# Kernel tuning notes

Measured on AMD Instinct MI355X. Metric: run time of the kernel, lower is better.

The kernel has to match this reference:

```python
import jax, jax.numpy as jnp
import numpy as np

B, N, D = 1, 2048, 2048
H, DH, DR, MP = 16, 128, 64, 4
LOCAL = H * DH // MP  # per-shard qkv width
ATTN_MASK_VALUE = -1e10
LN_EPS = 1e-5


def setup_inputs() -> dict:
    key = jax.random.key(0)
    ks = jax.random.split(key, 5)
    s = 0.02
    return {
        "x": jax.random.normal(ks[0], (B, N, D), jnp.float32),
        "ln_scale": jnp.ones((D,), jnp.float32),
        "ln_offset": jnp.zeros((D,), jnp.float32),
        "w_qkv": jax.random.normal(ks[1], (D, 3 * H * DH), jnp.float32) * s,
        "w_attn_out": jax.random.normal(ks[2], (H * DH, D), jnp.float32) * s,
        "w_ff_in": jax.random.normal(ks[3], (D, 4 * D), jnp.float32) * s,
        "b_ff_in": jnp.zeros((4 * D,), jnp.float32),
        "w_ff_out": jax.random.normal(ks[4], (4 * D, D), jnp.float32) * s,
        "b_ff_out": jnp.zeros((D,), jnp.float32),
    }


def _rotate_every_two(x):
    # (..., d) -> interleaved (-x2, x1) pairs, GPT-J style
    x1 = x[..., ::2]
    x2 = x[..., 1::2]
    return jnp.stack((-x2, x1), axis=-1).reshape(x.shape)


def _fixed_pos_embedding(n, dim):
    inv_freq = 1.0 / (10000.0 ** (np.arange(0, dim, 2, dtype=np.float32) / dim))
    ang = np.einsum("i,j->ij", np.arange(n, dtype=np.float32), inv_freq)  # [n, dim/2]
    return jnp.asarray(np.sin(ang), jnp.float32), jnp.asarray(np.cos(ang), jnp.float32)


def _apply_rotary(x, sin, cos):
    # x: [b, n, h, d_rot]; sin/cos: [n, d_rot/2] repeated pairwise -> [1, n, 1, d_rot]
    sin = jnp.repeat(sin, 2, axis=-1)[None, :, None, :]
    cos = jnp.repeat(cos, 2, axis=-1)[None, :, None, :]
    return x * cos + _rotate_every_two(x) * sin


def reference(x, ln_scale, ln_offset, w_qkv, w_attn_out, w_ff_in, b_ff_in, w_ff_out, b_ff_out):
    # ---- LayerNorm (shared input to parallel attn + FFN) ----
    mu = jnp.mean(x, axis=-1, keepdims=True)
    var = jnp.var(x, axis=-1, keepdims=True)
    h = (x - mu) * jax.lax.rsqrt(var + LN_EPS) * ln_scale + ln_offset

    # ---- Causal self-attention with partial rotary ----
    qkv = (h @ w_qkv).reshape(B, N, MP, 3 * LOCAL)  # mp-sharded layout
    q, v, k = jnp.split(qkv, [LOCAL, 2 * LOCAL], axis=-1)
    heads = lambda t: t.reshape(B, N, H, DH)  # shard_heads: [b,n,mp,local] -> [b,n,h,dh]
    q, v, k = heads(q), heads(v), heads(k)

    sin, cos = _fixed_pos_embedding(N, DR)
    q = jnp.concatenate([_apply_rotary(q[..., :DR], sin, cos), q[..., DR:]], axis=-1)
    k = jnp.concatenate([_apply_rotary(k[..., :DR], sin, cos), k[..., DR:]], axis=-1)

    attn_scale = np.float32(np.sqrt(DH))
    logits = jnp.einsum("bihd,bjhd->bhij", q, k) / attn_scale
    causal_mask = jnp.triu(jnp.ones((N, N), dtype=bool), 1)
    logits = jnp.where(causal_mask, ATTN_MASK_VALUE, logits)
    attn_w = jax.nn.softmax(logits, axis=-1)
    attn_vec = jnp.einsum("bhij,bjhd->bihd", attn_w, v).reshape(B, N, H * DH)
    attn_out = attn_vec @ w_attn_out

    # ---- FFN (parallel branch, same LN input) ----
    ff_out = jax.nn.gelu(h @ w_ff_in + b_ff_in) @ w_ff_out + b_ff_out

    return attn_out + ff_out
```

## Files before the change

### kernel.cpp

```cpp
#include <hip/hip_runtime.h>
#include <hip/hip_bf16.h>

using bf16_t = __hip_bfloat16;
typedef __attribute__((ext_vector_type(8))) __bf16 bfrag;
typedef __attribute__((ext_vector_type(4))) float f32x4;

#define MFMA16(a, b, c) __builtin_amdgcn_mfma_f32_16x16x32_bf16((a), (b), (c), 0, 0, 0)

__device__ __forceinline__ void gload_lds16(const void* g, void* l) {
  __builtin_amdgcn_global_load_lds((const __attribute__((address_space(1))) void*)g,
                                   (__attribute__((address_space(3))) void*)l, 16, 0, 0);
}

__device__ __forceinline__ float bf2f(unsigned u) { return __uint_as_float(u << 16); }

__global__ __launch_bounds__(256) void transpose_cvt(const float* __restrict__ in,
    bf16_t* __restrict__ out, int K, int N) {
  __shared__ float t[64][65];
  const int n0 = blockIdx.x * 64, k0 = blockIdx.y * 64;
  const int tx = threadIdx.x & 15, ty = threadIdx.x >> 4;
#pragma unroll
  for (int i = 0; i < 4; ++i) {
    float4 v = *(const float4*)&in[(size_t)(k0 + i * 16 + ty) * N + n0 + tx * 4];
    t[i * 16 + ty][tx * 4 + 0] = v.x; t[i * 16 + ty][tx * 4 + 1] = v.y;
    t[i * 16 + ty][tx * 4 + 2] = v.z; t[i * 16 + ty][tx * 4 + 3] = v.w;
  }
  __syncthreads();
#pragma unroll
  for (int i = 0; i < 4; ++i) {
    const int n = i * 16 + ty;
    bf16_t w[4];
#pragma unroll
    for (int j = 0; j < 4; ++j) w[j] = bf16_t(t[tx * 4 + j][n]);
    *(uint2*)&out[(size_t)(n0 + n) * K + k0 + tx * 4] = *(const uint2*)w;
  }
}

__global__ __launch_bounds__(256) void ln_kernel(const float* __restrict__ x,
    const float* __restrict__ sc, const float* __restrict__ of, bf16_t* __restrict__ h) {
  __shared__ float red[8];
  const int n = blockIdx.x, tid = threadIdx.x;
  const float* xr = x + (size_t)n * 2048;
  float4 a = ((const float4*)xr)[tid * 2];
  float4 b = ((const float4*)xr)[tid * 2 + 1];
  float s = a.x + a.y + a.z + a.w + b.x + b.y + b.z + b.w;
  float q = a.x * a.x + a.y * a.y + a.z * a.z + a.w * a.w +
            b.x * b.x + b.y * b.y + b.z * b.z + b.w * b.w;
#pragma unroll
  for (int m = 32; m; m >>= 1) { s += __shfl_xor(s, m); q += __shfl_xor(q, m); }
  if ((tid & 63) == 0) { red[(tid >> 6) * 2] = s; red[(tid >> 6) * 2 + 1] = q; }
  __syncthreads();
  s = red[0] + red[2] + red[4] + red[6];
  q = red[1] + red[3] + red[5] + red[7];
  const float mu = s * (1.f / 2048.f);
  const float inv = rsqrtf(q * (1.f / 2048.f) - mu * mu + 1e-5f);
  const int base = tid * 8;
  float v[8] = {a.x, a.y, a.z, a.w, b.x, b.y, b.z, b.w};
  bf16_t* hr = h + (size_t)n * 2048 + base;
#pragma unroll
  for (int j = 0; j < 8; ++j) hr[j] = bf16_t((v[j] - mu) * inv * sc[base + j] + of[base + j]);
}

template <int EPI>
__global__ __launch_bounds__(512, 2) void gemm2p(
    const bf16_t* __restrict__ A, int lda, const bf16_t* __restrict__ BT, int ldb,
    const float* __restrict__ bias, float* __restrict__ Cf, bf16_t* __restrict__ Cb,
    int M, int N, int K, size_t splitStride) {
  extern __shared__ __align__(16) char lds[];
  const int tid = threadIdx.x, wid = tid >> 6, lane = tid & 63;
  const int lc = lane & 15, lg = lane >> 4;
  const int bm = blockIdx.y * 256, bn = blockIdx.x * 256;
  const int wr = wid >> 2, wc = wid & 3;
  const int NT = K >> 6;
  const int sr = wid * 16 + (lane >> 2);
  const int lgp = (lane & 3) ^ ((sr >> 1) & 3);
  const size_t rA = (size_t)128 * lda, rB = (size_t)128 * ldb;
  const bf16_t* pA0 = A + (size_t)blockIdx.z * K + (size_t)(bm + sr) * lda + lgp * 8;
  const bf16_t* pA1 = pA0 + 32;
  const bf16_t* pB0 = BT + (size_t)blockIdx.z * K + (size_t)(bn + sr) * ldb + lgp * 8;
  const bf16_t* pB1 = pB0 + 32;
  auto stA0 = [&](int ts) { char* b = lds + (((ts & 1) * 2 + 0) << 14) + wid * 1024;
    gload_lds16(pA0, b); gload_lds16(pA0 + rA, b + 8192); pA0 += 64; };
  auto stA1 = [&](int ts) { char* b = lds + (((ts & 1) * 2 + 1) << 14) + wid * 1024;
    gload_lds16(pA1, b); gload_lds16(pA1 + rA, b + 8192); pA1 += 64; };
  auto stB0 = [&](int ts) { char* b = lds + 65536 + (((ts & 1) * 2 + 0) << 14) + wid * 1024;
    gload_lds16(pB0, b); gload_lds16(pB0 + rB, b + 8192); pB0 += 64; };
  auto stB1 = [&](int ts) { char* b = lds + 65536 + (((ts & 1) * 2 + 1) << 14) + wid * 1024;
    gload_lds16(pB1, b); gload_lds16(pB1 + rB, b + 8192); pB1 += 64; };

  stA0(0); stB0(0); stA1(0); stB1(0); stA0(1); stB0(1);
  asm volatile("s_waitcnt vmcnt(8)" ::: "memory");
  __builtin_amdgcn_s_barrier();

  f32x4 acc[8][4] = {};
#define FR(off, row) \
  (*(const bfrag*)(lds + (off) + (row) * 64 + ((lg ^ (((row) >> 1) & 3)) << 4)))

  for (int t = 0; t < NT; ++t) {
    const int d = t & 1;
    const int aoff0 = (d * 2 + 0) << 14, aoff1 = (d * 2 + 1) << 14;
    const int boff0 = 65536 + aoff0, boff1 = 65536 + aoff1;
    {
      bfrag a[8], b[4];
#pragma unroll
      for (int m = 0; m < 8; ++m) a[m] = FR(aoff0, wr * 128 + m * 16 + lc);
#pragma unroll
      for (int n = 0; n < 4; ++n) b[n] = FR(boff0, wc * 64 + n * 16 + lc);
      if (t + 1 < NT) { stA1(t + 1); stB1(t + 1); }
      __builtin_amdgcn_s_barrier();
      asm volatile("s_waitcnt lgkmcnt(0)" ::: "memory");
      __builtin_amdgcn_sched_barrier(0);
      __builtin_amdgcn_s_setprio(1);
#pragma unroll
      for (int m = 0; m < 8; ++m)
#pragma unroll
        for (int n = 0; n < 4; ++n) acc[m][n] = MFMA16(a[m], b[n], acc[m][n]);
      __builtin_amdgcn_s_setprio(0);
      if (t < NT - 2) asm volatile("s_waitcnt vmcnt(8)" ::: "memory");
      else            asm volatile("s_waitcnt vmcnt(0)" ::: "memory");
      __builtin_amdgcn_s_barrier();
    }
    {
      bfrag a[8], b[4];
#pragma unroll
      for (int m = 0; m < 8; ++m) a[m] = FR(aoff1, wr * 128 + m * 16 + lc);
#pragma unroll
      for (int n = 0; n < 4; ++n) b[n] = FR(boff1, wc * 64 + n * 16 + lc);
      if (t + 2 < NT) { stA0(t + 2); stB0(t + 2); }
      __builtin_amdgcn_s_barrier();
      asm volatile("s_waitcnt lgkmcnt(0)" ::: "memory");
      __builtin_amdgcn_sched_barrier(0);
      __builtin_amdgcn_s_setprio(1);
#pragma unroll
      for (int m = 0; m < 8; ++m)
#pragma unroll
        for (int n = 0; n < 4; ++n) acc[m][n] = MFMA16(a[m], b[n], acc[m][n]);
      __builtin_amdgcn_s_setprio(0);
      if (t < NT - 2) asm volatile("s_waitcnt vmcnt(8)" ::: "memory");
      else            asm volatile("s_waitcnt vmcnt(0)" ::: "memory");
      __builtin_amdgcn_s_barrier();
    }
  }
#undef FR
  char* W = lds + wid * 16384;
  if (EPI & 8) {
    bf16_t* Wb = (bf16_t*)W;
    bf16_t* Cbz = Cb + (size_t)blockIdx.z * splitStride;
#pragma unroll
    for (int mc = 0; mc < 2; ++mc) {
#pragma unroll
      for (int m4 = 0; m4 < 4; ++m4) {
#pragma unroll
        for (int n = 0; n < 4; ++n) {
          const int col = bn + wc * 64 + n * 16 + lc;
          float bv = (EPI & 1) ? bias[col] : 0.f;
#pragma unroll
          for (int i = 0; i < 4; ++i) {
            float v = acc[mc * 4 + m4][n][i];
            if (EPI & 1) v += bv;
            if (EPI & 2) v = 0.5f * v * (1.f + tanhf(0.7978845608028654f * (v + 0.044715f * v * v * v)));
            Wb[(m4 * 16 + lg * 4 + i) * 72 + n * 16 + lc] = bf16_t(v);
          }
        }
      }
      asm volatile("s_waitcnt lgkmcnt(0)" ::: "memory");
      __builtin_amdgcn_sched_barrier(0);
#pragma unroll
      for (int p = 0; p < 8; ++p) {
        const int rl = p * 8 + (lane >> 3), j = lane & 7;
        uint4 v = *(const uint4*)&Wb[rl * 72 + j * 8];
        const int grow = bm + wr * 128 + mc * 64 + rl;
        const int gcol = bn + wc * 64 + j * 8;
        *(uint4*)&Cbz[(size_t)grow * N + gcol] = v;
      }
      asm volatile("s_waitcnt lgkmcnt(0)" ::: "memory");
      __builtin_amdgcn_sched_barrier(0);
    }
  } else {
    float* Wf = (float*)W;
    float* Cfz = Cf + (size_t)blockIdx.z * splitStride;
#pragma unroll
    for (int mc = 0; mc < 4; ++mc) {
#pragma unroll
      for (int m2 = 0; m2 < 2; ++m2) {
#pragma unroll
        for (int n = 0; n < 4; ++n) {
          const int col = bn + wc * 64 + n * 16 + lc;
          float bv = (EPI & 1) ? bias[col] : 0.f;
#pragma unroll
          for (int i = 0; i < 4; ++i) {
            float v = acc[mc * 2 + m2][n][i];
            if (EPI & 1) v += bv;
            if (EPI & 2) v = 0.5f * v * (1.f + tanhf(0.7978845608028654f * (v + 0.044715f * v * v * v)));
            Wf[(m2 * 16 + lg * 4 + i) * 72 + n * 16 + lc] = v;
          }
        }
      }
      asm volatile("s_waitcnt lgkmcnt(0)" ::: "memory");
      __builtin_amdgcn_sched_barrier(0);
#pragma unroll
      for (int p = 0; p < 8; ++p) {
        const int rl = p * 4 + (lane >> 4), j = lane & 15;
        float4 v = *(const float4*)&Wf[rl * 72 + j * 4];
        const int grow = bm + wr * 128 + mc * 32 + rl;
        const int gcol = bn + wc * 64 + j * 4;
        *(float4*)&Cfz[(size_t)grow * N + gcol] = v;
      }
      asm volatile("s_waitcnt lgkmcnt(0)" ::: "memory");
      __builtin_amdgcn_sched_barrier(0);
    }
  }
}

template <int NP, bool ADDIN, bool BIAS>
__global__ __launch_bounds__(256) void reduceP(const float* __restrict__ p0,
    const float* __restrict__ p1, const float* __restrict__ p2,
    const float* __restrict__ p3, const float* __restrict__ bias,
    float* __restrict__ out, int total, int colmask) {
  const int i = (blockIdx.x * 256 + threadIdx.x) * 4;
  if (i >= total) return;
  float4 v = *(const float4*)(p0 + i);
  float4 w = *(const float4*)(p1 + i);
  v.x += w.x; v.y += w.y; v.z += w.z; v.w += w.w;
  if (NP == 4) {
    float4 u = *(const float4*)(p2 + i);
    float4 z = *(const float4*)(p3 + i);
    v.x += u.x + z.x; v.y += u.y + z.y; v.z += u.z + z.z; v.w += u.w + z.w;
  }
  if (BIAS) {
    float4 b = *(const float4*)(bias + (i & colmask));
    v.x += b.x; v.y += b.y; v.z += b.z; v.w += b.w;
  }
  if (ADDIN) {
    float4 o = *(const float4*)(out + i);
    v.x += o.x; v.y += o.y; v.z += o.z; v.w += o.w;
  }
  *(float4*)(out + i) = v;
}

__global__ __launch_bounds__(256) void reduce4b(const bf16_t* __restrict__ p0,
    const bf16_t* __restrict__ p1, const bf16_t* __restrict__ p2,
    const bf16_t* __restrict__ p3, float* __restrict__ out, int total) {
  const int i = (blockIdx.x * 256 + threadIdx.x) * 8;
  if (i >= total) return;
  uint4 a0 = *(const uint4*)(p0 + i);
  uint4 a1 = *(const uint4*)(p1 + i);
  uint4 a2 = *(const uint4*)(p2 + i);
  uint4 a3 = *(const uint4*)(p3 + i);
  const unsigned* u0 = (const unsigned*)&a0;
  const unsigned* u1 = (const unsigned*)&a1;
  const unsigned* u2 = (const unsigned*)&a2;
  const unsigned* u3 = (const unsigned*)&a3;
  float r[8];
#pragma unroll
  for (int j = 0; j < 8; ++j) {
    const int w = j >> 1, sh = (j & 1) * 16;
    r[j] = bf2f((u0[w] >> sh) & 0xffffu) + bf2f((u1[w] >> sh) & 0xffffu) +
           bf2f((u2[w] >> sh) & 0xffffu) + bf2f((u3[w] >> sh) & 0xffffu);
  }
  *(float4*)(out + i) = make_float4(r[0], r[1], r[2], r[3]);
  *(float4*)(out + i + 4) = make_float4(r[4], r[5], r[6], r[7]);
}

__global__ __launch_bounds__(128) void rope_kernel(const bf16_t* __restrict__ qkv,
    bf16_t* __restrict__ qh, bf16_t* __restrict__ kh, bf16_t* __restrict__ vT) {
  const int n = blockIdx.x, hh = blockIdx.y;
  const int d = threadIdx.x;
  const int mp = hh >> 2, hi = hh & 3;
  const bf16_t* row = qkv + (size_t)n * 6144 + mp * 1536 + hi * 128;
  float q = __bfloat162float(row[d]);
  float k = __bfloat162float(row[1024 + d]);
  if (d < 64) {
    const float ang = (float)n * powf(10000.f, -(float)(d & ~1) / 64.f);
    const float sn = sinf(ang), cs = cosf(ang);
    const float qp = __shfl_xor(q, 1), kp = __shfl_xor(k, 1);
    if (d & 1) { q = q * cs + qp * sn; k = k * cs + kp * sn; }
    else       { q = q * cs - qp * sn; k = k * cs - kp * sn; }
  }
  qh[((size_t)hh * 2048 + n) * 128 + d] = bf16_t(q * 0.08838834764831845f);
  kh[((size_t)hh * 2048 + n) * 128 + d] = bf16_t(k);
  vT[((size_t)hh * 128 + d) * 2048 + n] = row[512 + d];
}

__global__ __launch_bounds__(256) void attn_kernel(const bf16_t* __restrict__ qh,
    const bf16_t* __restrict__ kh, const bf16_t* __restrict__ vT,
    bf16_t* __restrict__ Op, float2* __restrict__ ml) {
  __shared__ alignas(16) char Kbuf[2][16384];
  __shared__ alignas(16) char Vbuf[2][16384];
  __shared__ alignas(16) bf16_t Ps[4][16 * 72];
  const int p = blockIdx.x, h = blockIdx.y, z = blockIdx.z;
  const int tid = threadIdx.x, wid = tid >> 6, lane = tid & 63;
  const int lc = lane & 15, lg = lane >> 4;
  const int krow = wid * 4 + (lane >> 4);
  const int vrow = wid * 8 + (lane >> 3);

  auto stage = [&](int kv0, int d) {
#pragma unroll
    for (int i = 0; i < 4; ++i) {
      const int kr = i * 16 + krow;
      const int kch = (lane & 15) ^ (kr & 15);
      gload_lds16(kh + ((size_t)h * 2048 + kv0 + kr) * 128 + kch * 8,
                  Kbuf[d] + i * 4096 + wid * 1024);
      const int vr = i * 32 + vrow;
      const int vch = (lane & 7) ^ (vr & 7);
      gload_lds16(vT + ((size_t)h * 128 + vr) * 2048 + kv0 + vch * 8,
                  Vbuf[d] + i * 4096 + wid * 1024);
    }
  };
#define FRK(d, row, ch) (*(const bfrag*)(Kbuf[d] + (row) * 256 + (((ch) ^ ((row) & 15)) << 4)))
#define FRV(d, row, ch) (*(const bfrag*)(Vbuf[d] + (row) * 128 + (((ch) ^ ((row) & 7)) << 4)))

#pragma unroll 1
  for (int half = 0; half < 2; ++half) {
    const int qt = half ? (31 - p) : p;
    const int nkv = qt + 1;
    const int lo = (z * nkv) / 3, hi = ((z + 1) * nkv) / 3;
    const int nj = hi - lo;
    const int qr = qt * 64 + wid * 16;
    const bf16_t* Qb = qh + ((size_t)h * 2048 + qr) * 128;
    bfrag qf[4];
#pragma unroll
    for (int ks = 0; ks < 4; ++ks)
      qf[ks] = *(const bfrag*)&Qb[lc * 128 + ks * 32 + lg * 8];
    f32x4 O[8] = {};
    float mr[4] = {-1e30f, -1e30f, -1e30f, -1e30f};
    float lsum[4] = {0.f, 0.f, 0.f, 0.f};

    if (nj > 0) {
      stage(lo * 64, 0);
      asm volatile("s_waitcnt vmcnt(0)" ::: "memory");
      __builtin_amdgcn_s_barrier();
    }
#pragma unroll 1
    for (int j = 0; j < nj; ++j) {
      const int kt = lo + j, d = j & 1;
      const int kv0 = kt * 64;
      if (j + 1 < nj) stage(kv0 + 64, d ^ 1);
      f32x4 s[4];
#pragma unroll
      for (int c = 0; c < 4; ++c) {
        f32x4 a = {};
#pragma unroll
        for (int ks = 0; ks < 4; ++ks) {
          bfrag kf = FRK(d, c * 16 + lc, ks * 4 + lg);
          a = MFMA16(qf[ks], kf, a);
        }
        s[c] = a;
      }
      if (kt == qt) {
#pragma unroll
        for (int c = 0; c < 4; ++c)
#pragma unroll
          for (int i = 0; i < 4; ++i)
            if (kv0 + c * 16 + lc > qr + lg * 4 + i) s[c][i] = -1e10f;
      }
      float pm[4];
#pragma unroll
      for (int i = 0; i < 4; ++i)
        pm[i] = fmaxf(fmaxf(s[0][i], s[1][i]), fmaxf(s[2][i], s[3][i]));
#pragma unroll
      for (int m = 1; m < 16; m <<= 1)
#pragma unroll
        for (int i = 0; i < 4; ++i) pm[i] = fmaxf(pm[i], __shfl_xor(pm[i], m));
      float al[4], rs[4];
#pragma unroll
      for (int i = 0; i < 4; ++i) {
        const float mn = fmaxf(mr[i], pm[i]);
        al[i] = __expf(mr[i] - mn);
        mr[i] = mn;
        rs[i] = 0.f;
      }
#pragma unroll
      for (int c = 0; c < 4; ++c)
#pragma unroll
        for (int i = 0; i < 4; ++i) {
          const float pv = __expf(s[c][i] - mr[i]);
          s[c][i] = pv; rs[i] += pv;
        }
#pragma unroll
      for (int m = 1; m < 16; m <<= 1)
#pragma unroll
        for (int i = 0; i < 4; ++i) rs[i] += __shfl_xor(rs[i], m);
#pragma unroll
      for (int i = 0; i < 4; ++i) lsum[i] = lsum[i] * al[i] + rs[i];
#pragma unroll
      for (int n = 0; n < 8; ++n)
#pragma unroll
        for (int i = 0; i < 4; ++i) O[n][i] *= al[i];
#pragma unroll
      for (int c = 0; c < 4; ++c)
#pragma unroll
        for (int i = 0; i < 4; ++i)
          Ps[wid][(lg * 4 + i) * 72 + c * 16 + lc] = bf16_t(s[c][i]);
#pragma unroll
      for (int k2 = 0; k2 < 2; ++k2) {
        bfrag pf = *(const bfrag*)((const char*)&Ps[wid][0] + lc * 144 + k2 * 64 + lg * 16);
#pragma unroll
        for (int n = 0; n < 8; ++n) {
          bfrag vf = FRV(d, n * 16 + lc, k2 * 4 + lg);
          O[n] = MFMA16(pf, vf, O[n]);
        }
      }
      if (j + 1 < nj) asm volatile("s_waitcnt vmcnt(0)" ::: "memory");
      asm volatile("s_waitcnt lgkmcnt(0)" ::: "memory");
      __builtin_amdgcn_s_barrier();
    }
    const size_t rb = (size_t)(z * 16 + h) * 2048 + qr;
#pragma unroll
    for (int n = 0; n < 8; ++n)
#pragma unroll
      for (int i = 0; i < 4; ++i)
        Op[(rb + lg * 4 + i) * 128 + n * 16 + lc] = bf16_t(O[n][i]);
    if (lc == 0) {
#pragma unroll
      for (int i = 0; i < 4; ++i)
        ml[rb + lg * 4 + i] = make_float2(mr[i], lsum[i]);
    }
    __builtin_amdgcn_s_barrier();
  }
#undef FRK
#undef FRV
}

__global__ __launch_bounds__(256) void attn_combine(const bf16_t* __restrict__ Op,
    const float2* __restrict__ ml, bf16_t* __restrict__ av) {
  const int idx = blockIdx.x * 256 + threadIdx.x;
  const int t = idx & 15, hr = idx >> 4;
  const int ZS = 16 * 2048;
  const size_t ZO = (size_t)ZS * 128;
  const float2 m0 = ml[hr], m1 = ml[ZS + hr], m2 = ml[2 * ZS + hr];
  const float M = fmaxf(fmaxf(m0.x, m1.x), m2.x);
  const float w0 = __expf(m0.x - M), w1 = __expf(m1.x - M), w2 = __expf(m2.x - M);
  const float inv = 1.f / (w0 * m0.y + w1 * m1.y + w2 * m2.y);
  const bf16_t* p0 = Op + (size_t)hr * 128 + t * 8;
  uint4 a0 = *(const uint4*)p0;
  uint4 a1 = *(const uint4*)(p0 + ZO);
  uint4 a2 = *(const uint4*)(p0 + 2 * ZO);
  const unsigned* u0 = (const unsigned*)&a0;
  const unsigned* u1 = (const unsigned*)&a1;
  const unsigned* u2 = (const unsigned*)&a2;
  bf16_t ov[8];
#pragma unroll
  for (int j = 0; j < 8; ++j) {
    const int w = j >> 1, sh = (j & 1) * 16;
    ov[j] = bf16_t((w0 * bf2f((u0[w] >> sh) & 0xffffu) +
                    w1 * bf2f((u1[w] >> sh) & 0xffffu) +
                    w2 * bf2f((u2[w] >> sh) & 0xffffu)) * inv);
  }
  const int row = hr & 2047, hh = hr >> 11;
  *(uint4*)(av + (size_t)row * 2048 + hh * 128 + t * 8) = *(const uint4*)ov;
}

extern "C" void kernel_launch(void* const* d_in, const int* in_sizes, int n_in,
                              void* d_out, int out_size, void* d_ws, size_t ws_size,
                              hipStream_t stream) {
  const float* x        = (const float*)d_in[0];
  const float* ln_scale = (const float*)d_in[1];
  const float* ln_offset= (const float*)d_in[2];
  const float* w_qkv    = (const float*)d_in[3];
  const float* w_ao     = (const float*)d_in[4];
  const float* w_ff_in  = (const float*)d_in[5];
  const float* b_ff_in  = (const float*)d_in[6];
  const float* w_ff_out = (const float*)d_in[7];
  const float* b_ff_out = (const float*)d_in[8];
  float* out = (float*)d_out;

  char* ws = (char*)d_ws;
  bf16_t* wqkvT   = (bf16_t*)(ws);
  bf16_t* waoT    = (bf16_t*)(ws + 25165824);
  bf16_t* wffinT  = (bf16_t*)(ws + 33554432);
  bf16_t* wffoutT = (bf16_t*)(ws + 67108864);
  bf16_t* h       = (bf16_t*)(ws + 100663296);
  bf16_t* qhb     = (bf16_t*)(ws + 109051904);
  bf16_t* khb     = (bf16_t*)(ws + 117440512);
  bf16_t* vTb     = (bf16_t*)(ws + 125829120);
  bf16_t* avb     = (bf16_t*)(ws + 134217728);
  bf16_t* qkvb    = (bf16_t*)(ws + 142606336);
  bf16_t* ff1b    = qkvb;
  bf16_t* pab     = qkvb;
  float*  pf      = (float*)(ws);
  bf16_t* Opart   = (bf16_t*)(ws);
  float2* mlpart  = (float2*)(ws + 167772160);

  hipFuncSetAttribute((const void*)gemm2p<0>,  hipFuncAttributeMaxDynamicSharedMemorySize, 131072);
  hipFuncSetAttribute((const void*)gemm2p<8>,  hipFuncAttributeMaxDynamicSharedMemorySize, 131072);
  hipFuncSetAttribute((const void*)gemm2p<11>, hipFuncAttributeMaxDynamicSharedMemorySize, 131072);

  dim3 b256(256), b512(512);
  transpose_cvt<<<dim3(96, 32),  b256, 0, stream>>>(w_qkv,    wqkvT,   2048, 6144);
  transpose_cvt<<<dim3(32, 32),  b256, 0, stream>>>(w_ao,     waoT,    2048, 2048);
  transpose_cvt<<<dim3(128, 32), b256, 0, stream>>>(w_ff_in,  wffinT,  2048, 8192);
  transpose_cvt<<<dim3(32, 128), b256, 0, stream>>>(w_ff_out, wffoutT, 8192, 2048);
  ln_kernel<<<dim3(2048), b256, 0, stream>>>(x, ln_scale, ln_offset, h);

  gemm2p<8><<<dim3(24, 8, 1), b512, 131072, stream>>>(h, 2048, wqkvT, 2048,
      nullptr, nullptr, qkvb, 2048, 6144, 2048, 0);
  rope_kernel<<<dim3(2048, 16), dim3(128), 0, stream>>>(qkvb, qhb, khb, vTb);

  attn_kernel<<<dim3(16, 16, 3), b256, 0, stream>>>(qhb, khb, vTb, Opart, mlpart);
  attn_combine<<<dim3(2048), b256, 0, stream>>>(Opart, mlpart, avb);

  gemm2p<8><<<dim3(8, 8, 4), b512, 131072, stream>>>(avb, 2048, waoT, 2048,
      nullptr, nullptr, pab, 2048, 2048, 512, (size_t)2048 * 2048);
  reduce4b<<<dim3(2048), b256, 0, stream>>>(pab, pab + 4194304, pab + 2 * 4194304,
      pab + 3 * 4194304, out, 4194304);

  gemm2p<11><<<dim3(32, 8, 1), b512, 131072, stream>>>(h, 2048, wffinT, 2048,
      b_ff_in, nullptr, ff1b, 2048, 8192, 2048, 0);

  gemm2p<0><<<dim3(8, 8, 4), b512, 131072, stream>>>(ff1b, 8192, wffoutT, 8192,
      nullptr, pf, nullptr, 2048, 2048, 2048, (size_t)2048 * 2048);
  reduceP<4, true, true><<<dim3(4096), b256, 0, stream>>>(pf, pf + 4194304,
      pf + 2 * 4194304, pf + 3 * 4194304, b_ff_out, out, 4194304, 2047);
}
```

Before: 421.8 us.

## Restructure GEMM main loop into 8-phase schedule with quarter-tile LDS staging

Replaces the two-phase-per-k-tile GEMM loop with an eight-phase schedule. Each phase loads a quarter of the A/B fragments, issues one half-tile global->LDS load, and runs 16 MFMAs between barriers. The LDS layout changes from two 32-column halves to full 64-column rows with an XOR swizzle over 8 chunks. The aim is to interleave global loads, LDS reads and MFMAs more finely, hiding memory latency with fewer registers live per phase. The cost is many more barriers per k-tile.

```diff
diff --git a/kernel.cpp b/kernel.cpp
--- a/kernel.cpp
+++ b/kernel.cpp
@@ -62,7 +62,7 @@
 }
 
 template <int EPI>
-__global__ __launch_bounds__(512, 2) void gemm2p(
+__global__ __launch_bounds__(512, 2) void gemm8p(
     const bf16_t* __restrict__ A, int lda, const bf16_t* __restrict__ BT, int ldb,
     const float* __restrict__ bias, float* __restrict__ Cf, bf16_t* __restrict__ Cb,
     int M, int N, int K, size_t splitStride) {
@@ -71,77 +71,110 @@
   const int lc = lane & 15, lg = lane >> 4;
   const int bm = blockIdx.y * 256, bn = blockIdx.x * 256;
   const int wr = wid >> 2, wc = wid & 3;
-  const int NT = K >> 6;
-  const int sr = wid * 16 + (lane >> 2);
-  const int lgp = (lane & 3) ^ ((sr >> 1) & 3);
-  const size_t rA = (size_t)128 * lda, rB = (size_t)128 * ldb;
-  const bf16_t* pA0 = A + (size_t)blockIdx.z * K + (size_t)(bm + sr) * lda + lgp * 8;
-  const bf16_t* pA1 = pA0 + 32;
-  const bf16_t* pB0 = BT + (size_t)blockIdx.z * K + (size_t)(bn + sr) * ldb + lgp * 8;
-  const bf16_t* pB1 = pB0 + 32;
-  auto stA0 = [&](int ts) { char* b = lds + (((ts & 1) * 2 + 0) << 14) + wid * 1024;
-    gload_lds16(pA0, b); gload_lds16(pA0 + rA, b + 8192); pA0 += 64; };
-  auto stA1 = [&](int ts) { char* b = lds + (((ts & 1) * 2 + 1) << 14) + wid * 1024;
-    gload_lds16(pA1, b); gload_lds16(pA1 + rA, b + 8192); pA1 += 64; };
-  auto stB0 = [&](int ts) { char* b = lds + 65536 + (((ts & 1) * 2 + 0) << 14) + wid * 1024;
-    gload_lds16(pB0, b); gload_lds16(pB0 + rB, b + 8192); pB0 += 64; };
-  auto stB1 = [&](int ts) { char* b = lds + 65536 + (((ts & 1) * 2 + 1) << 14) + wid * 1024;
-    gload_lds16(pB1, b); gload_lds16(pB1 + rB, b + 8192); pB1 += 64; };
-
-  stA0(0); stB0(0); stA1(0); stB1(0); stA0(1); stB0(1);
-  asm volatile("s_waitcnt vmcnt(8)" ::: "memory");
+  const int NT = K >> 6, niter = NT >> 1;
+  const int srow = tid >> 3;
+  const int scol = (((tid & 7) ^ ((tid >> 3) & 7)) << 3);
+  const bf16_t* Abase = A + (size_t)blockIdx.z * K + (size_t)(bm + srow) * lda + scol;
+  const bf16_t* Bbase = BT + (size_t)blockIdx.z * K + (size_t)(bn + srow) * ldb + scol;
+  auto SA = [&](int T, int h) {
+    char* dst = lds + (T & 1) * 32768 + h * 16384 + wid * 1024;
+    const bf16_t* src = Abase + (size_t)(h * 128) * lda + T * 64;
+    gload_lds16(src, dst); gload_lds16(src + (size_t)64 * lda, dst + 8192);
+  };
+  auto SB = [&](int T, int h) {
+    char* dst = lds + 65536 + (T & 1) * 32768 + h * 16384 + wid * 1024;
+    const bf16_t* src = Bbase + (size_t)(h * 128) * ldb + T * 64;
+    gload_lds16(src, dst); gload_lds16(src + (size_t)64 * ldb, dst + 8192);
+  };
+#define FRA(d, row, kk) (*(const bfrag*)(lds + (d) * 32768 + wr * 16384 + (row) * 128 + \
+    ((((kk) * 4 + lg) ^ ((row) & 7)) << 4)))
+#define FRB(d, row, kk) (*(const bfrag*)(lds + 65536 + (d) * 32768 + (wc >> 1) * 16384 + \
+    (row) * 128 + ((((kk) * 4 + lg) ^ ((row) & 7)) << 4)))
+#define PHASE_SYNC() do { __builtin_amdgcn_s_barrier(); \
+    asm volatile("s_waitcnt lgkmcnt(0)" ::: "memory"); \
+    __builtin_amdgcn_sched_barrier(0); __builtin_amdgcn_s_setprio(1); } while (0)
+#define PHASE_END() do { __builtin_amdgcn_s_setprio(0); __builtin_amdgcn_s_barrier(); } while (0)
+#define PHASE_END_VM(lastf) do { __builtin_amdgcn_s_setprio(0); \
+    if (lastf) asm volatile("s_waitcnt vmcnt(0)" ::: "memory"); \
+    else       asm volatile("s_waitcnt vmcnt(4)" ::: "memory"); \
+    __builtin_amdgcn_s_barrier(); } while (0)
+
+  SB(0, 0); SB(0, 1); SA(0, 0); SA(0, 1); SB(1, 0); SB(1, 1);
+  asm volatile("s_waitcnt vmcnt(4)" ::: "memory");
   __builtin_amdgcn_s_barrier();
 
   f32x4 acc[8][4] = {};
-#define FR(off, row) \
-  (*(const bfrag*)(lds + (off) + (row) * 64 + ((lg ^ (((row) >> 1) & 3)) << 4)))
-
-  for (int t = 0; t < NT; ++t) {
-    const int d = t & 1;
-    const int aoff0 = (d * 2 + 0) << 14, aoff1 = (d * 2 + 1) << 14;
-    const int boff0 = 65536 + aoff0, boff1 = 65536 + aoff1;
-    {
-      bfrag a[8], b[4];
-#pragma unroll
-      for (int m = 0; m < 8; ++m) a[m] = FR(aoff0, wr * 128 + m * 16 + lc);
-#pragma unroll
-      for (int n = 0; n < 4; ++n) b[n] = FR(boff0, wc * 64 + n * 16 + lc);
-      if (t + 1 < NT) { stA1(t + 1); stB1(t + 1); }
-      __builtin_amdgcn_s_barrier();
-      asm volatile("s_waitcnt lgkmcnt(0)" ::: "memory");
-      __builtin_amdgcn_sched_barrier(0);
-      __builtin_amdgcn_s_setprio(1);
-#pragma unroll
-      for (int m = 0; m < 8; ++m)
-#pragma unroll
-        for (int n = 0; n < 4; ++n) acc[m][n] = MFMA16(a[m], b[n], acc[m][n]);
-      __builtin_amdgcn_s_setprio(0);
-      if (t < NT - 2) asm volatile("s_waitcnt vmcnt(8)" ::: "memory");
-      else            asm volatile("s_waitcnt vmcnt(0)" ::: "memory");
-      __builtin_amdgcn_s_barrier();
-    }
-    {
-      bfrag a[8], b[4];
-#pragma unroll
-      for (int m = 0; m < 8; ++m) a[m] = FR(aoff1, wr * 128 + m * 16 + lc);
-#pragma unroll
-      for (int n = 0; n < 4; ++n) b[n] = FR(boff1, wc * 64 + n * 16 + lc);
-      if (t + 2 < NT) { stA0(t + 2); stB0(t + 2); }
-      __builtin_amdgcn_s_barrier();
-      asm volatile("s_waitcnt lgkmcnt(0)" ::: "memory");
-      __builtin_amdgcn_sched_barrier(0);
-      __builtin_amdgcn_s_setprio(1);
-#pragma unroll
-      for (int m = 0; m < 8; ++m)
-#pragma unroll
-        for (int n = 0; n < 4; ++n) acc[m][n] = MFMA16(a[m], b[n], acc[m][n]);
-      __builtin_amdgcn_s_setprio(0);
-      if (t < NT - 2) asm volatile("s_waitcnt vmcnt(8)" ::: "memory");
-      else            asm volatile("s_waitcnt vmcnt(0)" ::: "memory");
-      __builtin_amdgcn_s_barrier();
-    }
-  }
-#undef FR
+  const int brl = (wc & 1) * 64 + lc;
+
+  for (int k = 0; k < niter; ++k) {
+    const int T1 = 2 * k + 1, T2 = 2 * k + 2, T3 = 2 * k + 3;
+    const bool last = (k == niter - 1);
+    bfrag aq[4][2], b01[2][2], b23[2][2];
+#pragma unroll 1
+    for (int d = 0; d < 2; ++d) {
+#pragma unroll
+      for (int m = 0; m < 4; ++m)
+#pragma unroll
+        for (int kk = 0; kk < 2; ++kk) aq[m][kk] = FRA(d, m * 16 + lc, kk);
+#pragma unroll
+      for (int n = 0; n < 2; ++n)
+#pragma unroll
+        for (int kk = 0; kk < 2; ++kk) b01[n][kk] = FRB(d, brl + n * 16, kk);
+      if (d == 0) SA(T1, 0); else if (!last) SA(T2, 0);
+      PHASE_SYNC();
+#pragma unroll
+      for (int kk = 0; kk < 2; ++kk)
+#pragma unroll
+        for (int m = 0; m < 4; ++m) {
+          acc[m][0] = MFMA16(aq[m][kk], b01[0][kk], acc[m][0]);
+          acc[m][1] = MFMA16(aq[m][kk], b01[1][kk], acc[m][1]);
+        }
+      PHASE_END();
+#pragma unroll
+      for (int n = 0; n < 2; ++n)
+#pragma unroll
+        for (int kk = 0; kk < 2; ++kk) b23[n][kk] = FRB(d, brl + (n + 2) * 16, kk);
+      if (d == 0) SA(T1, 1); else if (!last) SA(T2, 1);
+      PHASE_SYNC();
+#pragma unroll
+      for (int kk = 0; kk < 2; ++kk)
+#pragma unroll
+        for (int m = 0; m < 4; ++m) {
+          acc[m][2] = MFMA16(aq[m][kk], b23[0][kk], acc[m][2]);
+          acc[m][3] = MFMA16(aq[m][kk], b23[1][kk], acc[m][3]);
+        }
+      PHASE_END();
+#pragma unroll
+      for (int m = 0; m < 4; ++m)
+#pragma unroll
+        for (int kk = 0; kk < 2; ++kk) aq[m][kk] = FRA(d, (m + 4) * 16 + lc, kk);
+      if (!last) { if (d == 0) SB(T2, 0); else SB(T3, 0); }
+      PHASE_SYNC();
+#pragma unroll
+      for (int kk = 0; kk < 2; ++kk)
+#pragma unroll
+        for (int m = 0; m < 4; ++m) {
+          acc[4 + m][2] = MFMA16(aq[m][kk], b23[0][kk], acc[4 + m][2]);
+          acc[4 + m][3] = MFMA16(aq[m][kk], b23[1][kk], acc[4 + m][3]);
+        }
+      PHASE_END();
+      if (!last) { if (d == 0) SB(T2, 1); else SB(T3, 1); }
+      PHASE_SYNC();
+#pragma unroll
+      for (int kk = 0; kk < 2; ++kk)
+#pragma unroll
+        for (int m = 0; m < 4; ++m) {
+          acc[4 + m][0] = MFMA16(aq[m][kk], b01[0][kk], acc[4 + m][0]);
+          acc[4 + m][1] = MFMA16(aq[m][kk], b01[1][kk], acc[4 + m][1]);
+        }
+      PHASE_END_VM(last);
+    }
+  }
+#undef FRA
+#undef FRB
+#undef PHASE_SYNC
+#undef PHASE_END
+#undef PHASE_END_VM
   char* W = lds + wid * 16384;
   if (EPI & 8) {
     bf16_t* Wb = (bf16_t*)W;
@@ -482,9 +515,9 @@
   bf16_t* Opart   = (bf16_t*)(ws);
   float2* mlpart  = (float2*)(ws + 167772160);
 
-  hipFuncSetAttribute((const void*)gemm2p<0>,  hipFuncAttributeMaxDynamicSharedMemorySize, 131072);
-  hipFuncSetAttribute((const void*)gemm2p<8>,  hipFuncAttributeMaxDynamicSharedMemorySize, 131072);
-  hipFuncSetAttribute((const void*)gemm2p<11>, hipFuncAttributeMaxDynamicSharedMemorySize, 131072);
+  hipFuncSetAttribute((const void*)gemm8p<0>,  hipFuncAttributeMaxDynamicSharedMemorySize, 131072);
+  hipFuncSetAttribute((const void*)gemm8p<8>,  hipFuncAttributeMaxDynamicSharedMemorySize, 131072);
+  hipFuncSetAttribute((const void*)gemm8p<11>, hipFuncAttributeMaxDynamicSharedMemorySize, 131072);
 
   dim3 b256(256), b512(512);
   transpose_cvt<<<dim3(96, 32),  b256, 0, stream>>>(w_qkv,    wqkvT,   2048, 6144);
@@ -493,22 +526,22 @@
   transpose_cvt<<<dim3(32, 128), b256, 0, stream>>>(w_ff_out, wffoutT, 8192, 2048);
   ln_kernel<<<dim3(2048), b256, 0, stream>>>(x, ln_scale, ln_offset, h);
 
-  gemm2p<8><<<dim3(24, 8, 1), b512, 131072, stream>>>(h, 2048, wqkvT, 2048,
+  gemm8p<8><<<dim3(24, 8, 1), b512, 131072, stream>>>(h, 2048, wqkvT, 2048,
       nullptr, nullptr, qkvb, 2048, 6144, 2048, 0);
   rope_kernel<<<dim3(2048, 16), dim3(128), 0, stream>>>(qkvb, qhb, khb, vTb);
 
   attn_kernel<<<dim3(16, 16, 3), b256, 0, stream>>>(qhb, khb, vTb, Opart, mlpart);
   attn_combine<<<dim3(2048), b256, 0, stream>>>(Opart, mlpart, avb);
 
-  gemm2p<8><<<dim3(8, 8, 4), b512, 131072, stream>>>(avb, 2048, waoT, 2048,
+  gemm8p<8><<<dim3(8, 8, 4), b512, 131072, stream>>>(avb, 2048, waoT, 2048,
       nullptr, nullptr, pab, 2048, 2048, 512, (size_t)2048 * 2048);
   reduce4b<<<dim3(2048), b256, 0, stream>>>(pab, pab + 4194304, pab + 2 * 4194304,
       pab + 3 * 4194304, out, 4194304);
 
-  gemm2p<11><<<dim3(32, 8, 1), b512, 131072, stream>>>(h, 2048, wffinT, 2048,
+  gemm8p<11><<<dim3(32, 8, 1), b512, 131072, stream>>>(h, 2048, wffinT, 2048,
       b_ff_in, nullptr, ff1b, 2048, 8192, 2048, 0);
 
-  gemm2p<0><<<dim3(8, 8, 4), b512, 131072, stream>>>(ff1b, 8192, wffoutT, 8192,
+  gemm8p<0><<<dim3(8, 8, 4), b512, 131072, stream>>>(ff1b, 8192, wffoutT, 8192,
       nullptr, pf, nullptr, 2048, 2048, 2048, (size_t)2048 * 2048);
   reduceP<4, true, true><<<dim3(4096), b256, 0, stream>>>(pf, pf + 4194304,
       pf + 2 * 4194304, pf + 3 * 4194304, b_ff_out, out, 4194304, 2047);
```

Measured after the change: 416.6 us. About the same (-1.2%).
